# Kernel tuning notes

Hardware: AMD Instinct MI355X
Metric: run time of the kernel (lower is better)

The kernel has to match this reference:

```python
import jax, jax.numpy as jnp
import numpy as np

N_NODES = 100000
N_EDGES = 600000
DIM_IN = 128
DIM_H = 128
DIM_OUT = 64
N_LAYERS = 3
BN_EPS = 1e-5


def setup_inputs() -> dict:
    key = jax.random.key(0)
    ks = jax.random.split(key, 10)
    x = jax.random.normal(ks[0], (N_NODES, DIM_IN), dtype=jnp.float32)
    edge_index = jax.random.randint(ks[1], (2, N_EDGES), 0, N_NODES, dtype=jnp.int64)
    s = 0.05
    conv_w1 = jax.random.normal(ks[2], (N_LAYERS, DIM_H, DIM_H), dtype=jnp.float32) * s
    conv_b1 = jnp.zeros((N_LAYERS, DIM_H), jnp.float32)
    conv_w2 = jax.random.normal(ks[3], (N_LAYERS, DIM_H, DIM_H), dtype=jnp.float32) * s
    conv_b2 = jnp.zeros((N_LAYERS, DIM_H), jnp.float32)
    bn_gamma = jnp.ones((N_LAYERS, DIM_H), jnp.float32)
    bn_beta = jnp.zeros((N_LAYERS, DIM_H), jnp.float32)
    fc1_w = jax.random.normal(ks[4], (DIM_H, DIM_H), dtype=jnp.float32) * s
    fc1_b = jnp.zeros((DIM_H,), jnp.float32)
    fc2_w = jax.random.normal(ks[5], (DIM_H, DIM_OUT), dtype=jnp.float32) * s
    fc2_b = jnp.zeros((DIM_OUT,), jnp.float32)
    # deterministic dropout mask, p=0.5, inverted-dropout scaling baked in (0 or 2)
    dropout_mask = (jax.random.uniform(ks[6], (N_NODES, DIM_H)) < 0.5).astype(jnp.float32) * 2.0
    return {"x": x, "edge_index": edge_index,
            "conv_w1": conv_w1, "conv_b1": conv_b1, "conv_w2": conv_w2, "conv_b2": conv_b2,
            "bn_gamma": bn_gamma, "bn_beta": bn_beta,
            "fc1_w": fc1_w, "fc1_b": fc1_b, "fc2_w": fc2_w, "fc2_b": fc2_b,
            "dropout_mask": dropout_mask}


def reference(x, edge_index, conv_w1, conv_b1, conv_w2, conv_b2,
              bn_gamma, bn_beta, fc1_w, fc1_b, fc2_w, fc2_b, dropout_mask):
    src, dst = edge_index[0], edge_index[1]
    n = x.shape[0]
    h = x
    for l in range(N_LAYERS):
        # GINConv (eps=0): (1+eps)*h + sum_{j->i} h_j, then 2-layer MLP
        agg = h + jax.ops.segment_sum(h[src], dst, num_segments=n)
        z = jnp.maximum(agg @ conv_w1[l] + conv_b1[l], 0.0) @ conv_w2[l] + conv_b2[l]
        z = jnp.maximum(z, 0.0)  # outer ReLU
        # BatchNorm1d (training mode: batch stats, biased variance)
        mean = z.mean(axis=0)
        var = z.var(axis=0)
        h = (z - mean) * jax.lax.rsqrt(var + BN_EPS) * bn_gamma[l] + bn_beta[l]
    h = jnp.maximum(h @ fc1_w + fc1_b, 0.0)
    h = h * dropout_mask  # dropout p=0.5 with precomputed inverted mask
    logits = h @ fc2_w + fc2_b
    return jax.nn.log_softmax(logits, axis=-1)
```

## Files before the change

kernel.cpp:

```cpp
#include <hip/hip_runtime.h>
#include <stdint.h>

#define N_NODES 100000
#define N_EDGES 600000
#define DIM_H   128
#define DIM_OUT 64
#define WPAD    136
#define BN_EPS  1e-5f
#define NBLK    391
#define GRID64_HEAD 1563
#define MLP_GRID 782

typedef __attribute__((ext_vector_type(8))) __bf16        bh8;
typedef __attribute__((ext_vector_type(4))) float         fl4;
typedef __attribute__((ext_vector_type(8))) unsigned short us8;
typedef __attribute__((ext_vector_type(4))) unsigned short us4;

__device__ __forceinline__ unsigned short f2bfbits(float f) {
  unsigned int u = __builtin_bit_cast(unsigned int, f);
  u += 0x7fffu + ((u >> 16) & 1u);
  return (unsigned short)(u >> 16);
}
__device__ __forceinline__ float bf2f(unsigned short b) {
  unsigned int u = ((unsigned int)b) << 16;
  return __builtin_bit_cast(float, u);
}
__device__ __forceinline__ void wave_lds_fence() {
  asm volatile("s_waitcnt lgkmcnt(0)" ::: "memory");
  __builtin_amdgcn_sched_barrier(0);
}

__global__ void prep_kernel(const float* __restrict__ cw1, const float* __restrict__ cw2,
                            const float* __restrict__ fc1w, const float* __restrict__ fc2w,
                            unsigned short* __restrict__ W1F, unsigned short* __restrict__ W2F,
                            unsigned short* __restrict__ F1F, unsigned short* __restrict__ F2F,
                            float* __restrict__ stats, int* __restrict__ deg,
                            unsigned short* __restrict__ zrow) {
  int t = blockIdx.x * 256 + threadIdx.x;
  if (t < 3 * 16384) {
    int l = t >> 14, o = t & 16383;
    int j = o & 7, lane = (o >> 3) & 63, kk = (o >> 9) & 3, n0 = o >> 11;
    int k = kk * 32 + ((lane >> 4) << 3) + j;
    int n = (n0 << 4) + (lane & 15);
    W1F[t] = f2bfbits(cw1[l * 16384 + k * 128 + n]);
    W2F[t] = f2bfbits(cw2[l * 16384 + k * 128 + n]);
  }
  if (t < 16384) {
    int o = t;
    int j = o & 7, lane = (o >> 3) & 63, kk = (o >> 9) & 3, n0 = o >> 11;
    int k = kk * 32 + ((lane >> 4) << 3) + j;
    int n = (n0 << 4) + (lane & 15);
    F1F[t] = f2bfbits(fc1w[k * 128 + n]);
  }
  if (t < 8192) {
    int o = t;
    int j = o & 7, lane = (o >> 3) & 63, kk = (o >> 9) & 3, n0 = o >> 11;
    int k = kk * 32 + ((lane >> 4) << 3) + j;
    int n = (n0 << 4) + (lane & 15);
    F2F[t] = f2bfbits(fc2w[k * 64 + n]);
  }
  if (t < 768)   stats[t] = 0.f;
  if (t < 128)   zrow[t] = 0;
  if (t < N_NODES) deg[t] = 0;
}

__global__ void deg_xcast(const float* __restrict__ x, unsigned short* __restrict__ xB,
                          const int* __restrict__ ei, int* __restrict__ deg,
                          const float* __restrict__ mask, unsigned int* __restrict__ bmask) {
  int i = blockIdx.x * 256 + threadIdx.x;
  fl4 v = reinterpret_cast<const fl4*>(x)[i];
  us4 p;
#pragma unroll
  for (int j = 0; j < 4; ++j) p[j] = f2bfbits(v[j]);
  reinterpret_cast<us4*>(xB)[i] = p;
  if (i < N_EDGES) atomicAdd(&deg[ei[N_EDGES + i]], 1);
  if (i < N_NODES * 4) {
    const float* mp = mask + (long)i * 32;
    unsigned int b = 0;
#pragma unroll
    for (int j8 = 0; j8 < 8; ++j8) {
      fl4 mv = *reinterpret_cast<const fl4*>(mp + j8 * 4);
      b |= (mv[0] > 0.f ? 1u : 0u) << (j8 * 4 + 0);
      b |= (mv[1] > 0.f ? 1u : 0u) << (j8 * 4 + 1);
      b |= (mv[2] > 0.f ? 1u : 0u) << (j8 * 4 + 2);
      b |= (mv[3] > 0.f ? 1u : 0u) << (j8 * 4 + 3);
    }
    bmask[i] = b;
  }
}

__global__ void scanA(const int* __restrict__ deg, int* __restrict__ rowstart,
                      int* __restrict__ bsum) {
  __shared__ int s[256];
  int t = threadIdx.x, i = blockIdx.x * 256 + t;
  int v = (i < N_NODES) ? deg[i] : 0;
  s[t] = v;
  __syncthreads();
#pragma unroll
  for (int off = 1; off < 256; off <<= 1) {
    int u = (t >= off) ? s[t - off] : 0;
    __syncthreads();
    s[t] += u;
    __syncthreads();
  }
  if (i < N_NODES) rowstart[i] = s[t] - v;
  if (t == 0) bsum[blockIdx.x] = s[255];
}

__global__ void scanC(int* __restrict__ rowstart, const int* __restrict__ bsum,
                      int* __restrict__ cursor) {
  __shared__ int sred[256];
  int b = blockIdx.x, t = threadIdx.x;
  int partial = 0;
  for (int j = t; j < b; j += 256) partial += bsum[j];
  sred[t] = partial;
  __syncthreads();
#pragma unroll
  for (int off = 128; off > 0; off >>= 1) {
    if (t < off) sred[t] += sred[t + off];
    __syncthreads();
  }
  int boffb = sred[0];
  int i = b * 256 + t;
  if (i < N_NODES) {
    int v = rowstart[i] + boffb;
    rowstart[i] = v;
    cursor[i] = v;
  }
  if (i == 0) rowstart[N_NODES] = N_EDGES;
}

__global__ void csr_fill(const int* __restrict__ ei, int* __restrict__ cursor,
                         int* __restrict__ csr_src) {
  int e = blockIdx.x * 256 + threadIdx.x;
  if (e < N_EDGES) {
    int pos = atomicAdd(&cursor[ei[N_EDGES + e]], 1);
    csr_src[pos] = ei[e];
  }
}

__global__ void bn_finalize(const float* __restrict__ stats, const float* __restrict__ gamma,
                            const float* __restrict__ beta, float* __restrict__ sb) {
  int c = threadIdx.x;
  const float inv_n = 1.0f / (float)N_NODES;
  float mean = stats[c] * inv_n;
  float var  = stats[128 + c] * inv_n - mean * mean;
  float s = gamma[c] * rsqrtf(var + BN_EPS);
  sb[c] = s;
  sb[128 + c] = beta[c] - mean * s;
}

template <int AFFINE>
__global__ __launch_bounds__(256)
void gather_h(const unsigned short* __restrict__ H, const float* __restrict__ sb,
              const int* __restrict__ rowstart, const int* __restrict__ csr,
              unsigned short* __restrict__ aggB) {
  int node = blockIdx.x * 4 + (threadIdx.x >> 6);
  int lane = threadIdx.x & 63;
  int q = lane >> 4, lc = lane & 15;
  int c = lc * 8;

  fl4 scA, scB, bcA, bcB;
  if (AFFINE) {
    scA = *reinterpret_cast<const fl4*>(sb + c);
    scB = *reinterpret_cast<const fl4*>(sb + c + 4);
    bcA = *reinterpret_cast<const fl4*>(sb + 128 + c);
    bcB = *reinterpret_cast<const fl4*>(sb + 128 + c + 4);
  }

  int nodeu = __builtin_amdgcn_readfirstlane(node);
  int rs = rowstart[nodeu], re = rowstart[nodeu + 1];
  int cnt = re - rs + 1;
  float acc[8] = {0.f, 0.f, 0.f, 0.f, 0.f, 0.f, 0.f, 0.f};

  for (int base = 0; base < cnt; base += 64) {
    int item = base + lane;
    int myidx = (item == 0) ? nodeu
              : ((item < cnt) ? csr[rs + item - 1] : N_NODES);
    int lim = cnt - base; if (lim > 64) lim = 64;
    for (int sub = 0; sub < lim; sub += 8) {
      int i0 = __shfl(myidx, sub + q);
      int i1 = __shfl(myidx, sub + 4 + q);
      us8 r0 = *reinterpret_cast<const us8*>(H + (long)i0 * DIM_H + c);
      us8 r1 = *reinterpret_cast<const us8*>(H + (long)i1 * DIM_H + c);
#pragma unroll
      for (int j = 0; j < 8; ++j) acc[j] += bf2f(r0[j]) + bf2f(r1[j]);
    }
  }

#pragma unroll
  for (int j = 0; j < 8; ++j) {
    acc[j] += __shfl_xor(acc[j], 16);
    acc[j] += __shfl_xor(acc[j], 32);
  }

  if (q == 0) {
    us8 pk;
    if (AFFINE) {
      float fc = (float)cnt;
#pragma unroll
      for (int j = 0; j < 4; ++j) {
        pk[j]     = f2bfbits(scA[j] * acc[j]     + fc * bcA[j]);
        pk[4 + j] = f2bfbits(scB[j] * acc[4 + j] + fc * bcB[j]);
      }
    } else {
#pragma unroll
      for (int j = 0; j < 8; ++j) pk[j] = f2bfbits(acc[j]);
    }
    *reinterpret_cast<us8*>(aggB + (long)node * DIM_H + c) = pk;
  }
}

__global__ __launch_bounds__(256, 2)
void mlp_kernel(const unsigned short* __restrict__ A,
                const unsigned short* __restrict__ W1F, const float* __restrict__ b1,
                const unsigned short* __restrict__ W2F, const float* __restrict__ b2,
                unsigned short* __restrict__ Z, float* __restrict__ stats) {
  __shared__ __align__(16) unsigned short wbuf[16384];
  __shared__ __align__(16) unsigned short ybuf[128 * WPAD];
  __shared__ float red[4][2][128];

  const int tid = threadIdx.x;
  const int wid = tid >> 6, lane = tid & 63;
  const int lr = lane & 15, lg = lane >> 4;
  const int row0 = blockIdx.x * 128;

  bh8 afrag[2][4];
#pragma unroll
  for (int rt = 0; rt < 2; ++rt) {
    int row = row0 + wid * 32 + rt * 16 + lr;
    bool valid = row < N_NODES;
    const unsigned short* ap = A + (long)row * DIM_H;
#pragma unroll
    for (int kk = 0; kk < 4; ++kk) {
      us8 t = (us8)0;
      if (valid) t = *reinterpret_cast<const us8*>(ap + kk * 32 + 8 * lg);
      afrag[rt][kk] = __builtin_bit_cast(bh8, t);
    }
  }

#pragma unroll
  for (int i = 0; i < 8; ++i) {
    int ch = i * 256 + tid;
    *reinterpret_cast<uint4*>(&wbuf[ch * 8]) = *reinterpret_cast<const uint4*>(&W1F[ch * 8]);
  }
  __syncthreads();

#pragma unroll
  for (int n0 = 0; n0 < 8; ++n0) {
    fl4 acc[2] = {{0,0,0,0},{0,0,0,0}};
#pragma unroll
    for (int kk = 0; kk < 4; ++kk) {
      bh8 b = *reinterpret_cast<const bh8*>(&wbuf[((n0 * 4 + kk) << 9) + lane * 8]);
      acc[0] = __builtin_amdgcn_mfma_f32_16x16x32_bf16(afrag[0][kk], b, acc[0], 0, 0, 0);
      acc[1] = __builtin_amdgcn_mfma_f32_16x16x32_bf16(afrag[1][kk], b, acc[1], 0, 0, 0);
    }
    float bias = b1[n0 * 16 + lr];
#pragma unroll
    for (int rt = 0; rt < 2; ++rt)
#pragma unroll
      for (int r = 0; r < 4; ++r) {
        float v = acc[rt][r] + bias;
        v = v > 0.f ? v : 0.f;
        ybuf[(wid * 32 + rt * 16 + 4 * lg + r) * WPAD + n0 * 16 + lr] = f2bfbits(v);
      }
  }

  __syncthreads();

#pragma unroll
  for (int i = 0; i < 8; ++i) {
    int ch = i * 256 + tid;
    *reinterpret_cast<uint4*>(&wbuf[ch * 8]) = *reinterpret_cast<const uint4*>(&W2F[ch * 8]);
  }

  bh8 a2[2][4];
#pragma unroll
  for (int rt = 0; rt < 2; ++rt)
#pragma unroll
    for (int kk = 0; kk < 4; ++kk)
      a2[rt][kk] = *reinterpret_cast<const bh8*>(
          &ybuf[(wid * 32 + rt * 16 + lr) * WPAD + kk * 32 + 8 * lg]);

  __syncthreads();

#pragma unroll
  for (int n0 = 0; n0 < 8; ++n0) {
    fl4 acc[2] = {{0,0,0,0},{0,0,0,0}};
#pragma unroll
    for (int kk = 0; kk < 4; ++kk) {
      bh8 b = *reinterpret_cast<const bh8*>(&wbuf[((n0 * 4 + kk) << 9) + lane * 8]);
      acc[0] = __builtin_amdgcn_mfma_f32_16x16x32_bf16(a2[0][kk], b, acc[0], 0, 0, 0);
      acc[1] = __builtin_amdgcn_mfma_f32_16x16x32_bf16(a2[1][kk], b, acc[1], 0, 0, 0);
    }
    float bias = b2[n0 * 16 + lr];
    float sp = 0.f, qp = 0.f;
#pragma unroll
    for (int rt = 0; rt < 2; ++rt)
#pragma unroll
      for (int r = 0; r < 4; ++r) {
        int row = row0 + wid * 32 + rt * 16 + 4 * lg + r;
        float v = acc[rt][r] + bias;
        v = v > 0.f ? v : 0.f;
        ybuf[(wid * 32 + rt * 16 + 4 * lg + r) * WPAD + n0 * 16 + lr] = f2bfbits(v);
        if (row < N_NODES) { sp += v; qp += v * v; }
      }
    sp += __shfl_xor(sp, 16); sp += __shfl_xor(sp, 32);
    qp += __shfl_xor(qp, 16); qp += __shfl_xor(qp, 32);
    if (lg == 0) { red[wid][0][n0 * 16 + lr] = sp; red[wid][1][n0 * 16 + lr] = qp; }
  }

  wave_lds_fence();

#pragma unroll
  for (int i = 0; i < 8; ++i) {
    int ch = i * 64 + lane;
    int r  = wid * 32 + (ch >> 4);
    int c8 = (ch & 15) << 3;
    int row = row0 + r;
    if (row < N_NODES)
      *reinterpret_cast<uint4*>(&Z[(long)row * DIM_H + c8]) =
          *reinterpret_cast<const uint4*>(&ybuf[r * WPAD + c8]);
  }

  __syncthreads();

  {
    int which = tid >> 7, cc = tid & 127;
    float v = red[0][which][cc] + red[1][which][cc] + red[2][which][cc] + red[3][which][cc];
    unsafeAtomicAdd(&stats[which * 128 + cc], v);
  }
}

__global__ __launch_bounds__(256, 6)
void head_kernel(const unsigned short* __restrict__ Z, const float* __restrict__ sb,
                 const unsigned short* __restrict__ F1F, const float* __restrict__ fc1b,
                 const unsigned short* __restrict__ F2F, const float* __restrict__ fc2b,
                 const unsigned int* __restrict__ bmask, float* __restrict__ out) {
  __shared__ __align__(16) unsigned short ybuf[64 * WPAD];

  const int tid = threadIdx.x;
  const int wid = tid >> 6, lane = tid & 63;
  const int lr = lane & 15, lg = lane >> 4;
  const int row0 = blockIdx.x * 64;

  unsigned int bw[4][4];
#pragma unroll
  for (int r = 0; r < 4; ++r) {
    int row = row0 + wid * 16 + 4 * lg + r;
    if (row < N_NODES) {
      uint4 t = *reinterpret_cast<const uint4*>(bmask + (long)row * 4);
      bw[r][0] = t.x; bw[r][1] = t.y; bw[r][2] = t.z; bw[r][3] = t.w;
    } else {
      bw[r][0] = bw[r][1] = bw[r][2] = bw[r][3] = 0u;
    }
  }

  bh8 afrag[4];
#pragma unroll
  for (int kk = 0; kk < 4; ++kk) {
    int k0 = kk * 32 + 8 * lg;
    fl4 s0  = *reinterpret_cast<const fl4*>(sb + k0);
    fl4 s1  = *reinterpret_cast<const fl4*>(sb + k0 + 4);
    fl4 bb0 = *reinterpret_cast<const fl4*>(sb + 128 + k0);
    fl4 bb1 = *reinterpret_cast<const fl4*>(sb + 128 + k0 + 4);
    int row = row0 + wid * 16 + lr;
    us8 t = (us8)0;
    if (row < N_NODES) {
      us8 zv = *reinterpret_cast<const us8*>(Z + (long)row * DIM_H + k0);
#pragma unroll
      for (int j = 0; j < 4; ++j) {
        t[j]     = f2bfbits(bf2f(zv[j])     * s0[j] + bb0[j]);
        t[4 + j] = f2bfbits(bf2f(zv[4 + j]) * s1[j] + bb1[j]);
      }
    }
    afrag[kk] = __builtin_bit_cast(bh8, t);
  }

#pragma unroll
  for (int n0 = 0; n0 < 8; ++n0) {
    fl4 acc = {0.f, 0.f, 0.f, 0.f};
#pragma unroll
    for (int kk = 0; kk < 4; ++kk) {
      bh8 b = *reinterpret_cast<const bh8*>(&F1F[((n0 * 4 + kk) << 9) + lane * 8]);
      acc = __builtin_amdgcn_mfma_f32_16x16x32_bf16(afrag[kk], b, acc, 0, 0, 0);
    }
    float bias = fc1b[n0 * 16 + lr];
#pragma unroll
    for (int r = 0; r < 4; ++r) {
      float v = acc[r] + bias;
      v = v > 0.f ? v : 0.f;
      float mk = ((bw[r][n0 >> 1] >> (((n0 & 1) << 4) + lr)) & 1u) ? 2.0f : 0.0f;
      ybuf[(wid * 16 + 4 * lg + r) * WPAD + n0 * 16 + lr] = f2bfbits(v * mk);
    }
  }
  wave_lds_fence();

  bh8 a2[4];
#pragma unroll
  for (int kk = 0; kk < 4; ++kk)
    a2[kk] = *reinterpret_cast<const bh8*>(
        &ybuf[(wid * 16 + lr) * WPAD + kk * 32 + 8 * lg]);

  fl4 acc2[4];
#pragma unroll
  for (int n0 = 0; n0 < 4; ++n0) {
    acc2[n0] = (fl4){0.f, 0.f, 0.f, 0.f};
#pragma unroll
    for (int kk = 0; kk < 4; ++kk) {
      bh8 b = *reinterpret_cast<const bh8*>(&F2F[((n0 * 4 + kk) << 9) + lane * 8]);
      acc2[n0] = __builtin_amdgcn_mfma_f32_16x16x32_bf16(a2[kk], b, acc2[n0], 0, 0, 0);
    }
    float bias = fc2b[n0 * 16 + lr];
#pragma unroll
    for (int r = 0; r < 4; ++r) acc2[n0][r] += bias;
  }

#pragma unroll
  for (int r = 0; r < 4; ++r) {
    float m = fmaxf(fmaxf(acc2[0][r], acc2[1][r]), fmaxf(acc2[2][r], acc2[3][r]));
#pragma unroll
    for (int d = 1; d < 16; d <<= 1) m = fmaxf(m, __shfl_xor(m, d, 16));
    float se = 0.f;
#pragma unroll
    for (int n0 = 0; n0 < 4; ++n0) se += __expf(acc2[n0][r] - m);
#pragma unroll
    for (int d = 1; d < 16; d <<= 1) se += __shfl_xor(se, d, 16);
    float lse = m + __logf(se);
    int row = row0 + wid * 16 + 4 * lg + r;
    if (row < N_NODES) {
#pragma unroll
      for (int n0 = 0; n0 < 4; ++n0)
        out[(long)row * DIM_OUT + n0 * 16 + lr] = acc2[n0][r] - lse;
    }
  }
}

extern "C" void kernel_launch(void* const* d_in, const int* in_sizes, int n_in,
                              void* d_out, int out_size, void* d_ws, size_t ws_size,
                              hipStream_t stream) {
  const float* x      = (const float*)d_in[0];
  const int*   ei     = (const int*)d_in[1];
  const float* cw1    = (const float*)d_in[2];
  const float* cb1    = (const float*)d_in[3];
  const float* cw2    = (const float*)d_in[4];
  const float* cb2    = (const float*)d_in[5];
  const float* gamma  = (const float*)d_in[6];
  const float* beta   = (const float*)d_in[7];
  const float* fc1w   = (const float*)d_in[8];
  const float* fc1b   = (const float*)d_in[9];
  const float* fc2w   = (const float*)d_in[10];
  const float* fc2b   = (const float*)d_in[11];
  const float* mask   = (const float*)d_in[12];
  float* out = (float*)d_out;

  char* ws = (char*)d_ws;
  unsigned short* aggB  = (unsigned short*)ws;
  unsigned short* Zb    = (unsigned short*)(ws + 25600000);
  unsigned short* W1F   = (unsigned short*)(ws + 51200256);
  unsigned short* W2F   = (unsigned short*)(ws + 51298560);
  unsigned short* F1F   = (unsigned short*)(ws + 51396864);
  unsigned short* F2F   = (unsigned short*)(ws + 51429632);
  float*          stats = (float*)(ws + 51446016);
  int*            rowst = (int*)(ws + 51449088);
  int*            cursor= (int*)(ws + 51849092);
  int*            csr   = (int*)(ws + 52249092);
  int*            bsum  = (int*)(ws + 54649092);
  unsigned int*   bmask = (unsigned int*)(ws + 54650656);
  float*          sb    = (float*)(ws + 56250656);
  if (ws_size < 56253728u) return;

  prep_kernel<<<NBLK, 256, 0, stream>>>(cw1, cw2, fc1w, fc2w, W1F, W2F, F1F, F2F,
                                        stats, cursor, Zb + (long)N_NODES * DIM_H);
  deg_xcast<<<12500, 256, 0, stream>>>(x, Zb, ei, cursor, mask, bmask);

  scanA<<<NBLK, 256, 0, stream>>>(cursor, rowst, bsum);
  scanC<<<NBLK, 256, 0, stream>>>(rowst, bsum, cursor);
  csr_fill<<<2344, 256, 0, stream>>>(ei, cursor, csr);

  gather_h<0><<<25000, 256, 0, stream>>>(Zb, nullptr, rowst, csr, aggB);
  mlp_kernel<<<MLP_GRID, 256, 0, stream>>>(aggB, W1F, cb1, W2F, cb2, Zb, stats);
  bn_finalize<<<1, 128, 0, stream>>>(stats, gamma, beta, sb);

  gather_h<1><<<25000, 256, 0, stream>>>(Zb, sb, rowst, csr, aggB);
  mlp_kernel<<<MLP_GRID, 256, 0, stream>>>(aggB, W1F + 16384, cb1 + 128, W2F + 16384,
                                           cb2 + 128, Zb, stats + 256);
  bn_finalize<<<1, 128, 0, stream>>>(stats + 256, gamma + 128, beta + 128, sb + 256);

  gather_h<1><<<25000, 256, 0, stream>>>(Zb, sb + 256, rowst, csr, aggB);
  mlp_kernel<<<MLP_GRID, 256, 0, stream>>>(aggB, W1F + 32768, cb1 + 256, W2F + 32768,
                                           cb2 + 256, Zb, stats + 512);
  bn_finalize<<<1, 128, 0, stream>>>(stats + 512, gamma + 256, beta + 256, sb + 512);

  head_kernel<<<GRID64_HEAD, 256, 0, stream>>>(Zb, sb + 512,
                                               F1F, fc1b, F2F, fc2b, bmask, out);
}
```

Measured before the change: 311.1 us.

## Stream MLP weights from global into registers with prefetch instead of LDS staging

The MLP kernel no longer copies each 32KB weight matrix into shared memory behind block-wide barriers. Each wave now loads its B fragments straight from global/L2 into registers, prefetching the next column tile's weights while the current MFMAs run, and the __syncthreads calls become per-wave LDS fences. Biases are hoisted into registers up front, and the head kernel gets the same register prefetch. Dropping the 32KB wbuf lets launch_bounds rise to 4 blocks per CU, in exchange for more register pressure and more L2 traffic, since every wave re-reads the weights.

```diff
diff --git a/kernel.cpp b/kernel.cpp
--- a/kernel.cpp
+++ b/kernel.cpp
@@ -211,12 +211,11 @@
   }
 }
 
-__global__ __launch_bounds__(256, 2)
+__global__ __launch_bounds__(256, 4)
 void mlp_kernel(const unsigned short* __restrict__ A,
                 const unsigned short* __restrict__ W1F, const float* __restrict__ b1,
                 const unsigned short* __restrict__ W2F, const float* __restrict__ b2,
                 unsigned short* __restrict__ Z, float* __restrict__ stats) {
-  __shared__ __align__(16) unsigned short wbuf[16384];
   __shared__ __align__(16) unsigned short ybuf[128 * WPAD];
   __shared__ float red[4][2][128];
 
@@ -239,40 +238,46 @@
     }
   }
 
-#pragma unroll
-  for (int i = 0; i < 8; ++i) {
-    int ch = i * 256 + tid;
-    *reinterpret_cast<uint4*>(&wbuf[ch * 8]) = *reinterpret_cast<const uint4*>(&W1F[ch * 8]);
-  }
-  __syncthreads();
+  float bias1[8], bias2[8];
+#pragma unroll
+  for (int n0 = 0; n0 < 8; ++n0) { bias1[n0] = b1[n0 * 16 + lr]; bias2[n0] = b2[n0 * 16 + lr]; }
+
+  bh8 bnxt[4];
+#pragma unroll
+  for (int kk = 0; kk < 4; ++kk)
+    bnxt[kk] = *reinterpret_cast<const bh8*>(&W1F[(kk << 9) + lane * 8]);
 
 #pragma unroll
   for (int n0 = 0; n0 < 8; ++n0) {
+    bh8 bc[4];
+#pragma unroll
+    for (int kk = 0; kk < 4; ++kk) bc[kk] = bnxt[kk];
+    if (n0 < 7) {
+#pragma unroll
+      for (int kk = 0; kk < 4; ++kk)
+        bnxt[kk] = *reinterpret_cast<const bh8*>(&W1F[(((n0 + 1) * 4 + kk) << 9) + lane * 8]);
+    }
     fl4 acc[2] = {{0,0,0,0},{0,0,0,0}};
 #pragma unroll
     for (int kk = 0; kk < 4; ++kk) {
-      bh8 b = *reinterpret_cast<const bh8*>(&wbuf[((n0 * 4 + kk) << 9) + lane * 8]);
-      acc[0] = __builtin_amdgcn_mfma_f32_16x16x32_bf16(afrag[0][kk], b, acc[0], 0, 0, 0);
-      acc[1] = __builtin_amdgcn_mfma_f32_16x16x32_bf16(afrag[1][kk], b, acc[1], 0, 0, 0);
-    }
-    float bias = b1[n0 * 16 + lr];
+      acc[0] = __builtin_amdgcn_mfma_f32_16x16x32_bf16(afrag[0][kk], bc[kk], acc[0], 0, 0, 0);
+      acc[1] = __builtin_amdgcn_mfma_f32_16x16x32_bf16(afrag[1][kk], bc[kk], acc[1], 0, 0, 0);
+    }
 #pragma unroll
     for (int rt = 0; rt < 2; ++rt)
 #pragma unroll
       for (int r = 0; r < 4; ++r) {
-        float v = acc[rt][r] + bias;
+        float v = acc[rt][r] + bias1[n0];
         v = v > 0.f ? v : 0.f;
         ybuf[(wid * 32 + rt * 16 + 4 * lg + r) * WPAD + n0 * 16 + lr] = f2bfbits(v);
       }
   }
 
-  __syncthreads();
-
-#pragma unroll
-  for (int i = 0; i < 8; ++i) {
-    int ch = i * 256 + tid;
-    *reinterpret_cast<uint4*>(&wbuf[ch * 8]) = *reinterpret_cast<const uint4*>(&W2F[ch * 8]);
-  }
+#pragma unroll
+  for (int kk = 0; kk < 4; ++kk)
+    bnxt[kk] = *reinterpret_cast<const bh8*>(&W2F[(kk << 9) + lane * 8]);
+
+  wave_lds_fence();
 
   bh8 a2[2][4];
 #pragma unroll
@@ -282,25 +287,31 @@
       a2[rt][kk] = *reinterpret_cast<const bh8*>(
           &ybuf[(wid * 32 + rt * 16 + lr) * WPAD + kk * 32 + 8 * lg]);
 
-  __syncthreads();
+  wave_lds_fence();
 
 #pragma unroll
   for (int n0 = 0; n0 < 8; ++n0) {
+    bh8 bc[4];
+#pragma unroll
+    for (int kk = 0; kk < 4; ++kk) bc[kk] = bnxt[kk];
+    if (n0 < 7) {
+#pragma unroll
+      for (int kk = 0; kk < 4; ++kk)
+        bnxt[kk] = *reinterpret_cast<const bh8*>(&W2F[(((n0 + 1) * 4 + kk) << 9) + lane * 8]);
+    }
     fl4 acc[2] = {{0,0,0,0},{0,0,0,0}};
 #pragma unroll
     for (int kk = 0; kk < 4; ++kk) {
-      bh8 b = *reinterpret_cast<const bh8*>(&wbuf[((n0 * 4 + kk) << 9) + lane * 8]);
-      acc[0] = __builtin_amdgcn_mfma_f32_16x16x32_bf16(a2[0][kk], b, acc[0], 0, 0, 0);
-      acc[1] = __builtin_amdgcn_mfma_f32_16x16x32_bf16(a2[1][kk], b, acc[1], 0, 0, 0);
-    }
-    float bias = b2[n0 * 16 + lr];
+      acc[0] = __builtin_amdgcn_mfma_f32_16x16x32_bf16(a2[0][kk], bc[kk], acc[0], 0, 0, 0);
+      acc[1] = __builtin_amdgcn_mfma_f32_16x16x32_bf16(a2[1][kk], bc[kk], acc[1], 0, 0, 0);
+    }
     float sp = 0.f, qp = 0.f;
 #pragma unroll
     for (int rt = 0; rt < 2; ++rt)
 #pragma unroll
       for (int r = 0; r < 4; ++r) {
         int row = row0 + wid * 32 + rt * 16 + 4 * lg + r;
-        float v = acc[rt][r] + bias;
+        float v = acc[rt][r] + bias2[n0];
         v = v > 0.f ? v : 0.f;
         ybuf[(wid * 32 + rt * 16 + 4 * lg + r) * WPAD + n0 * 16 + lr] = f2bfbits(v);
         if (row < N_NODES) { sp += v; qp += v * v; }
@@ -355,6 +366,12 @@
       bw[r][0] = bw[r][1] = bw[r][2] = bw[r][3] = 0u;
     }
   }
+
+  float bias1[8], bias2[4];
+#pragma unroll
+  for (int n0 = 0; n0 < 8; ++n0) bias1[n0] = fc1b[n0 * 16 + lr];
+#pragma unroll
+  for (int n0 = 0; n0 < 4; ++n0) bias2[n0] = fc2b[n0 * 16 + lr];
 
   bh8 afrag[4];
 #pragma unroll
@@ -377,23 +394,37 @@
     afrag[kk] = __builtin_bit_cast(bh8, t);
   }
 
+  bh8 bnxt[4];
+#pragma unroll
+  for (int kk = 0; kk < 4; ++kk)
+    bnxt[kk] = *reinterpret_cast<const bh8*>(&F1F[(kk << 9) + lane * 8]);
 #pragma unroll
   for (int n0 = 0; n0 < 8; ++n0) {
+    bh8 bc[4];
+#pragma unroll
+    for (int kk = 0; kk < 4; ++kk) bc[kk] = bnxt[kk];
+    if (n0 < 7) {
+#pragma unroll
+      for (int kk = 0; kk < 4; ++kk)
+        bnxt[kk] = *reinterpret_cast<const bh8*>(&F1F[(((n0 + 1) * 4 + kk) << 9) + lane * 8]);
+    }
     fl4 acc = {0.f, 0.f, 0.f, 0.f};
 #pragma unroll
-    for (int kk = 0; kk < 4; ++kk) {
-      bh8 b = *reinterpret_cast<const bh8*>(&F1F[((n0 * 4 + kk) << 9) + lane * 8]);
-      acc = __builtin_amdgcn_mfma_f32_16x16x32_bf16(afrag[kk], b, acc, 0, 0, 0);
-    }
-    float bias = fc1b[n0 * 16 + lr];
+    for (int kk = 0; kk < 4; ++kk)
+      acc = __builtin_amdgcn_mfma_f32_16x16x32_bf16(afrag[kk], bc[kk], acc, 0, 0, 0);
 #pragma unroll
     for (int r = 0; r < 4; ++r) {
-      float v = acc[r] + bias;
+      float v = acc[r] + bias1[n0];
       v = v > 0.f ? v : 0.f;
       float mk = ((bw[r][n0 >> 1] >> (((n0 & 1) << 4) + lr)) & 1u) ? 2.0f : 0.0f;
       ybuf[(wid * 16 + 4 * lg + r) * WPAD + n0 * 16 + lr] = f2bfbits(v * mk);
     }
   }
+
+#pragma unroll
+  for (int kk = 0; kk < 4; ++kk)
+    bnxt[kk] = *reinterpret_cast<const bh8*>(&F2F[(kk << 9) + lane * 8]);
+
   wave_lds_fence();
 
   bh8 a2[4];
@@ -405,15 +436,20 @@
   fl4 acc2[4];
 #pragma unroll
   for (int n0 = 0; n0 < 4; ++n0) {
+    bh8 bc[4];
+#pragma unroll
+    for (int kk = 0; kk < 4; ++kk) bc[kk] = bnxt[kk];
+    if (n0 < 3) {
+#pragma unroll
+      for (int kk = 0; kk < 4; ++kk)
+        bnxt[kk] = *reinterpret_cast<const bh8*>(&F2F[(((n0 + 1) * 4 + kk) << 9) + lane * 8]);
+    }
     acc2[n0] = (fl4){0.f, 0.f, 0.f, 0.f};
 #pragma unroll
-    for (int kk = 0; kk < 4; ++kk) {
-      bh8 b = *reinterpret_cast<const bh8*>(&F2F[((n0 * 4 + kk) << 9) + lane * 8]);
-      acc2[n0] = __builtin_amdgcn_mfma_f32_16x16x32_bf16(a2[kk], b, acc2[n0], 0, 0, 0);
-    }
-    float bias = fc2b[n0 * 16 + lr];
-#pragma unroll
-    for (int r = 0; r < 4; ++r) acc2[n0][r] += bias;
+    for (int kk = 0; kk < 4; ++kk)
+      acc2[n0] = __builtin_amdgcn_mfma_f32_16x16x32_bf16(a2[kk], bc[kk], acc2[n0], 0, 0, 0);
+#pragma unroll
+    for (int r = 0; r < 4; ++r) acc2[n0][r] += bias2[n0];
   }
 
 #pragma unroll
```

After: 309.6 us. Within noise of the previous version (-0.5%).
